# Optimization experiments

Measured on AMD Instinct MI355X. Metric: run time of the kernel, lower is better.

The kernel has to match this reference:

```python
import jax, jax.numpy as jnp
import numpy as np

B, SQ, SKV, D = 8, 2048, 2048, 1024

def setup_inputs() -> dict:
    key = jax.random.key(0)
    ks = jax.random.split(key, 8)
    s = 1.0 / np.sqrt(D)  # torch Linear default init range
    return {
        "target": jax.random.normal(ks[0], (B, SQ, D), dtype=jnp.float32),
        "non_target": jax.random.normal(ks[1], (B, SKV, D), dtype=jnp.float32),
        "Wq": jax.random.uniform(ks[2], (D, D), jnp.float32, -s, s),
        "bq": jax.random.uniform(ks[3], (D,), jnp.float32, -s, s),
        "Wk": jax.random.uniform(ks[4], (D, D), jnp.float32, -s, s),
        "bk": jax.random.uniform(ks[5], (D,), jnp.float32, -s, s),
        "Wv": jax.random.uniform(ks[6], (D, D), jnp.float32, -s, s),
        "bv": jax.random.uniform(ks[7], (D,), jnp.float32, -s, s),
    }

def reference(target, non_target, Wq, bq, Wk, bk, Wv, bv):
    # Linear projections (torch Linear: x @ W.T + b)
    q = jnp.einsum('bsd,ed->bse', target, Wq) + bq       # [B,SQ,D]
    k = jnp.einsum('bsd,ed->bse', non_target, Wk) + bk   # [B,SKV,D]
    v = jnp.einsum('bsd,ed->bse', non_target, Wv) + bv   # [B,SKV,D]
    # Unscaled attention, exactly as the original module (no 1/sqrt(d))
    scores = jnp.einsum('bqd,bkd->bqk', q, k)            # [B,SQ,SKV]
    weights = jax.nn.softmax(scores, axis=-1)
    return jnp.einsum('bqk,bkd->bqd', weights, v)        # [B,SQ,D]
```

## Files before the change

### kernel.cpp

```cpp
#include <hip/hip_runtime.h>


typedef _Float16 half8 __attribute__((ext_vector_type(8)));
typedef _Float16 half4v __attribute__((ext_vector_type(4)));
typedef float floatx4 __attribute__((ext_vector_type(4)));

__device__ __forceinline__ void async_copy16(const _Float16* g, _Float16* l) {
  __builtin_amdgcn_global_load_lds(
      (const __attribute__((address_space(1))) void*)g,
      (__attribute__((address_space(3))) void*)l,
      16, 0, 0);
}

__global__ __launch_bounds__(256) void cast_f32_f16(const float* __restrict__ src,
                                                    _Float16* __restrict__ dst, long n) {
  long i = ((long)blockIdx.x * 256 + threadIdx.x) * 8;
  if (i >= n) return;
  float4 a = *(const float4*)(src + i);
  float4 b = *(const float4*)(src + i + 4);
  half8 h;
  h[0] = (_Float16)a.x; h[1] = (_Float16)a.y; h[2] = (_Float16)a.z; h[3] = (_Float16)a.w;
  h[4] = (_Float16)b.x; h[5] = (_Float16)b.y; h[6] = (_Float16)b.z; h[7] = (_Float16)b.w;
  *(half8*)(dst + i) = h;
}

template <int OMODE>
__global__ __launch_bounds__(256, 2) void gemm_bt(const _Float16* __restrict__ A,
                                                  const _Float16* __restrict__ B,
                                                  const float* __restrict__ bias,
                                                  void* __restrict__ out,
                                                  int K, int N,
                                                  long sA, long sB, long sO) {
  __shared__ __attribute__((aligned(16))) _Float16 As[128 * 64];
  __shared__ __attribute__((aligned(16))) _Float16 Bs[128 * 64];

  const int tid = threadIdx.x;
  const int lane = tid & 63;
  const int wave = tid >> 6;
  const long bz = blockIdx.z;

  const _Float16* Ab = A + bz * sA + (long)blockIdx.x * 128 * K;
  const _Float16* Bb = B + bz * sB + (long)blockIdx.y * 128 * K;

  const int wm = (wave & 1) * 64;
  const int wn = (wave >> 1) * 64;
  const int frow = lane & 15;
  const int fq = lane >> 4;
  const int fsw = frow & 7;

  floatx4 acc[4][4];
#pragma unroll
  for (int mt = 0; mt < 4; mt++)
#pragma unroll
    for (int nt = 0; nt < 4; nt++)
      acc[mt][nt] = (floatx4){0.f, 0.f, 0.f, 0.f};

  const int sr = tid >> 3;
  const int gl = (tid & 7) ^ (sr & 7);
  const long gOffBase = (long)sr * K + gl * 8;
  const int ldsOff = tid * 8;

  for (int k0 = 0; k0 < K; k0 += 64) {
    __syncthreads();
#pragma unroll
    for (int j = 0; j < 4; j++) {
      async_copy16(Ab + gOffBase + (long)(32 * j) * K + k0, As + ldsOff + j * 2048);
      async_copy16(Bb + gOffBase + (long)(32 * j) * K + k0, Bs + ldsOff + j * 2048);
    }
    __syncthreads();

#pragma unroll
    for (int h = 0; h < 2; h++) {
      half8 af[4], bf[4];
#pragma unroll
      for (int mt = 0; mt < 4; mt++)
        af[mt] = *(const half8*)(As + (wm + mt * 16 + frow) * 64 + ((h * 4 + fq) ^ fsw) * 8);
#pragma unroll
      for (int nt = 0; nt < 4; nt++)
        bf[nt] = *(const half8*)(Bs + (wn + nt * 16 + frow) * 64 + ((h * 4 + fq) ^ fsw) * 8);
#pragma unroll
      for (int mt = 0; mt < 4; mt++)
#pragma unroll
        for (int nt = 0; nt < 4; nt++)
          acc[mt][nt] = __builtin_amdgcn_mfma_f32_16x16x32_f16(af[mt], bf[nt], acc[mt][nt], 0, 0, 0);
    }
  }

  if (OMODE == 2 || OMODE == 3) {
#pragma unroll
    for (int nt = 0; nt < 4; nt++) {
      const int n = blockIdx.y * 128 + wn + nt * 16 + frow;
#pragma unroll
      for (int mt = 0; mt < 4; mt++) {
        const int rbase = blockIdx.x * 128 + wm + mt * 16 + fq * 4;
#pragma unroll
        for (int i = 0; i < 4; i++) {
          if (OMODE == 2)
            ((float*)out + bz * sO)[(long)(rbase + i) * N + n] = acc[mt][nt][i];
          else
            ((_Float16*)out + bz * sO)[(long)(rbase + i) * N + n] = (_Float16)acc[mt][nt][i];
        }
      }
    }
  } else {
#pragma unroll
    for (int nt = 0; nt < 4; nt++) {
      const int n = blockIdx.y * 128 + wn + nt * 16 + frow;
      const float bvv = bias[n];
#pragma unroll
      for (int mt = 0; mt < 4; mt++) {
        const int rbase = blockIdx.x * 128 + wm + mt * 16 + fq * 4;
        if (OMODE == 0) {
#pragma unroll
          for (int i = 0; i < 4; i++)
            ((_Float16*)out)[(long)(rbase + i) * N + n] = (_Float16)(acc[mt][nt][i] + bvv);
        } else {
          const long bb = rbase >> 11;
          const int s = rbase & 2047;
          half4v hv;
#pragma unroll
          for (int i = 0; i < 4; i++) hv[i] = (_Float16)(acc[mt][nt][i] + bvv);
          *(half4v*)((_Float16*)out + bb * (2048l * 1024) + (long)n * 2048 + s) = hv;
        }
      }
    }
  }
}

__global__ __launch_bounds__(256) void softmax_rows(const _Float16* __restrict__ S,
                                                    _Float16* __restrict__ P) {
  const long row = blockIdx.x;
  const _Float16* src = S + row * 2048;
  _Float16* dst = P + row * 2048;
  const int tid = threadIdx.x;

  half8 v = ((const half8*)src)[tid];
  float f[8];
#pragma unroll
  for (int i = 0; i < 8; i++) f[i] = (float)v[i];

  float m = fmaxf(fmaxf(fmaxf(f[0], f[1]), fmaxf(f[2], f[3])),
                  fmaxf(fmaxf(f[4], f[5]), fmaxf(f[6], f[7])));
#pragma unroll
  for (int o = 32; o > 0; o >>= 1) m = fmaxf(m, __shfl_xor(m, o, 64));
  __shared__ float redm[4];
  if ((tid & 63) == 0) redm[tid >> 6] = m;
  __syncthreads();
  m = fmaxf(fmaxf(redm[0], redm[1]), fmaxf(redm[2], redm[3]));

  float e[8], s = 0.f;
#pragma unroll
  for (int i = 0; i < 8; i++) { e[i] = __expf(f[i] - m); s += e[i]; }
#pragma unroll
  for (int o = 32; o > 0; o >>= 1) s += __shfl_xor(s, o, 64);
  __shared__ float reds[4];
  if ((tid & 63) == 0) reds[tid >> 6] = s;
  __syncthreads();
  s = (reds[0] + reds[1]) + (reds[2] + reds[3]);
  const float inv = 1.f / s;

  half8 h;
#pragma unroll
  for (int i = 0; i < 8; i++) h[i] = (_Float16)(e[i] * inv);
  ((half8*)dst)[tid] = h;
}

extern "C" void kernel_launch(void* const* d_in, const int* in_sizes, int n_in,
                              void* d_out, int out_size, void* d_ws, size_t ws_size,
                              hipStream_t stream) {
  const float* target = (const float*)d_in[0];
  const float* non_target = (const float*)d_in[1];
  const float* Wq = (const float*)d_in[2];
  const float* bq = (const float*)d_in[3];
  const float* Wk = (const float*)d_in[4];
  const float* bk = (const float*)d_in[5];
  const float* Wv = (const float*)d_in[6];
  const float* bv = (const float*)d_in[7];

  char* ws = (char*)d_ws;
  const size_t MB = 1ull << 20;
  _Float16* tgt16 = (_Float16*)(ws);
  _Float16* ntg16 = (_Float16*)(ws + 32 * MB);
  _Float16* S16 = (_Float16*)(ws);
  _Float16* P16 = (_Float16*)(ws + 64 * MB);
  _Float16* Q16 = (_Float16*)(ws + 128 * MB);
  _Float16* K16 = (_Float16*)(ws + 160 * MB);
  _Float16* Vt16 = (_Float16*)(ws + 192 * MB);
  _Float16* Wq16 = (_Float16*)(ws + 224 * MB);
  _Float16* Wk16 = (_Float16*)(ws + 226 * MB);
  _Float16* Wv16 = (_Float16*)(ws + 228 * MB);

  const long nBig = 8l * 2048 * 1024;
  const long nW = 1024l * 1024;

  cast_f32_f16<<<8192, 256, 0, stream>>>(target, tgt16, nBig);
  cast_f32_f16<<<8192, 256, 0, stream>>>(non_target, ntg16, nBig);
  cast_f32_f16<<<512, 256, 0, stream>>>(Wq, Wq16, nW);
  cast_f32_f16<<<512, 256, 0, stream>>>(Wk, Wk16, nW);
  cast_f32_f16<<<512, 256, 0, stream>>>(Wv, Wv16, nW);

  gemm_bt<0><<<dim3(128, 8, 1), 256, 0, stream>>>(tgt16, Wq16, bq, Q16, 1024, 1024, 0, 0, 0);
  gemm_bt<0><<<dim3(128, 8, 1), 256, 0, stream>>>(ntg16, Wk16, bk, K16, 1024, 1024, 0, 0, 0);
  gemm_bt<1><<<dim3(128, 8, 1), 256, 0, stream>>>(ntg16, Wv16, bv, Vt16, 1024, 1024, 0, 0, 0);

  gemm_bt<3><<<dim3(16, 16, 8), 256, 0, stream>>>(Q16, K16, nullptr, S16, 1024, 2048,
                                                  2048l * 1024, 2048l * 1024, 2048l * 2048);

  softmax_rows<<<16384, 256, 0, stream>>>(S16, P16);

  gemm_bt<2><<<dim3(16, 8, 8), 256, 0, stream>>>(P16, Vt16, nullptr, (float*)d_out, 2048, 1024,
                                                 2048l * 2048, 1024l * 2048, 2048l * 1024);
}
```

Measured before the change: 477.5 us.

## Fuse fp32-to-fp16 input cast into QKV projection GEMM and batch launches

```diff
diff --git a/kernel.cpp b/kernel.cpp
--- a/kernel.cpp
+++ b/kernel.cpp
@@ -12,22 +12,135 @@
       16, 0, 0);
 }
 
-__global__ __launch_bounds__(256) void cast_f32_f16(const float* __restrict__ src,
-                                                    _Float16* __restrict__ dst, long n) {
+__global__ __launch_bounds__(256) void cast_w(const float* __restrict__ Wq,
+                                              const float* __restrict__ Wk,
+                                              const float* __restrict__ Wv,
+                                              _Float16* __restrict__ dst) {
+  const float* src = blockIdx.y == 0 ? Wq : (blockIdx.y == 1 ? Wk : Wv);
+  const long base = (long)blockIdx.y * (1024l * 1024);
   long i = ((long)blockIdx.x * 256 + threadIdx.x) * 8;
-  if (i >= n) return;
   float4 a = *(const float4*)(src + i);
   float4 b = *(const float4*)(src + i + 4);
   half8 h;
   h[0] = (_Float16)a.x; h[1] = (_Float16)a.y; h[2] = (_Float16)a.z; h[3] = (_Float16)a.w;
   h[4] = (_Float16)b.x; h[5] = (_Float16)b.y; h[6] = (_Float16)b.z; h[7] = (_Float16)b.w;
-  *(half8*)(dst + i) = h;
+  *(half8*)(dst + base + i) = h;
+}
+
+__global__ __launch_bounds__(256, 2) void proj_fused(
+    const float* __restrict__ tgt, const float* __restrict__ ntg,
+    const _Float16* __restrict__ Wall,
+    const float* __restrict__ bq, const float* __restrict__ bk, const float* __restrict__ bv,
+    _Float16* __restrict__ QK16, _Float16* __restrict__ Vt16) {
+  constexpr int K = 1024, N = 1024;
+  __shared__ __attribute__((aligned(16))) _Float16 As[128 * 64];
+  __shared__ __attribute__((aligned(16))) _Float16 Bs[128 * 64];
+
+  const int tid = threadIdx.x;
+  const int lane = tid & 63;
+  const int wave = tid >> 6;
+  const int by = blockIdx.y;
+  const int mblk = blockIdx.x >> 3;
+  const int nblk = blockIdx.x & 7;
+
+  const float* Ag = (by == 0 ? tgt : ntg) + (long)mblk * 128 * K;
+  const _Float16* Bb = Wall + (long)by * (K * N) + (long)nblk * 128 * K;
+  const float* bias = (by == 0) ? bq : (by == 1 ? bk : bv);
+
+  const int wm = (wave & 1) * 64;
+  const int wn = (wave >> 1) * 64;
+  const int frow = lane & 15;
+  const int fq = lane >> 4;
+  const int fsw = frow & 7;
+
+  floatx4 acc[4][4];
+#pragma unroll
+  for (int mt = 0; mt < 4; mt++)
+#pragma unroll
+    for (int nt = 0; nt < 4; nt++)
+      acc[mt][nt] = (floatx4){0.f, 0.f, 0.f, 0.f};
+
+  const int sr = tid >> 3;
+  const int gl = (tid & 7) ^ (sr & 7);
+  const long gOff = (long)sr * K + gl * 8;
+  const int ldsOff = tid * 8;
+
+  for (int k0 = 0; k0 < K; k0 += 64) {
+    __syncthreads();
+#pragma unroll
+    for (int j = 0; j < 4; j++)
+      async_copy16(Bb + gOff + (long)(32 * j) * K + k0, Bs + ldsOff + j * 2048);
+    float4 u[4], w[4];
+#pragma unroll
+    for (int j = 0; j < 4; j++) {
+      const float4* ap = (const float4*)(Ag + gOff + (long)(32 * j) * K + k0);
+      u[j] = ap[0];
+      w[j] = ap[1];
+    }
+#pragma unroll
+    for (int j = 0; j < 4; j++) {
+      half8 h;
+      h[0] = (_Float16)u[j].x; h[1] = (_Float16)u[j].y;
+      h[2] = (_Float16)u[j].z; h[3] = (_Float16)u[j].w;
+      h[4] = (_Float16)w[j].x; h[5] = (_Float16)w[j].y;
+      h[6] = (_Float16)w[j].z; h[7] = (_Float16)w[j].w;
+      *(half8*)(As + ldsOff + j * 2048) = h;
+    }
+    __syncthreads();
+
+#pragma unroll
+    for (int h = 0; h < 2; h++) {
+      half8 af[4], bf[4];
+#pragma unroll
+      for (int mt = 0; mt < 4; mt++)
+        af[mt] = *(const half8*)(As + (wm + mt * 16 + frow) * 64 + ((h * 4 + fq) ^ fsw) * 8);
+#pragma unroll
+      for (int nt = 0; nt < 4; nt++)
+        bf[nt] = *(const half8*)(Bs + (wn + nt * 16 + frow) * 64 + ((h * 4 + fq) ^ fsw) * 8);
+#pragma unroll
+      for (int mt = 0; mt < 4; mt++)
+#pragma unroll
+        for (int nt = 0; nt < 4; nt++)
+          acc[mt][nt] = __builtin_amdgcn_mfma_f32_16x16x32_f16(af[mt], bf[nt], acc[mt][nt], 0, 0, 0);
+    }
+  }
+
+  if (by != 2) {
+    _Float16* O = QK16 + (long)by * (16l * 1024 * 1024);
+#pragma unroll
+    for (int nt = 0; nt < 4; nt++) {
+      const int n = nblk * 128 + wn + nt * 16 + frow;
+      const float bvv = bias[n];
+#pragma unroll
+      for (int mt = 0; mt < 4; mt++) {
+        const int rbase = mblk * 128 + wm + mt * 16 + fq * 4;
+#pragma unroll
+        for (int i = 0; i < 4; i++)
+          O[(long)(rbase + i) * N + n] = (_Float16)(acc[mt][nt][i] + bvv);
+      }
+    }
+  } else {
+#pragma unroll
+    for (int nt = 0; nt < 4; nt++) {
+      const int n = nblk * 128 + wn + nt * 16 + frow;
+      const float bvv = bias[n];
+#pragma unroll
+      for (int mt = 0; mt < 4; mt++) {
+        const int rbase = mblk * 128 + wm + mt * 16 + fq * 4;
+        const long bb = rbase >> 11;
+        const int s = rbase & 2047;
+        half4v hv;
+#pragma unroll
+        for (int i = 0; i < 4; i++) hv[i] = (_Float16)(acc[mt][nt][i] + bvv);
+        *(half4v*)(Vt16 + bb * (2048l * 1024) + (long)n * 2048 + s) = hv;
+      }
+    }
+  }
 }
 
 template <int OMODE>
 __global__ __launch_bounds__(256, 2) void gemm_bt(const _Float16* __restrict__ A,
                                                   const _Float16* __restrict__ B,
-                                                  const float* __restrict__ bias,
                                                   void* __restrict__ out,
                                                   int K, int N,
                                                   long sA, long sB, long sO) {
@@ -86,42 +199,18 @@
     }
   }
 
-  if (OMODE == 2 || OMODE == 3) {
-#pragma unroll
-    for (int nt = 0; nt < 4; nt++) {
-      const int n = blockIdx.y * 128 + wn + nt * 16 + frow;
-#pragma unroll
-      for (int mt = 0; mt < 4; mt++) {
-        const int rbase = blockIdx.x * 128 + wm + mt * 16 + fq * 4;
-#pragma unroll
-        for (int i = 0; i < 4; i++) {
-          if (OMODE == 2)
-            ((float*)out + bz * sO)[(long)(rbase + i) * N + n] = acc[mt][nt][i];
-          else
-            ((_Float16*)out + bz * sO)[(long)(rbase + i) * N + n] = (_Float16)acc[mt][nt][i];
-        }
-      }
-    }
-  } else {
-#pragma unroll
-    for (int nt = 0; nt < 4; nt++) {
-      const int n = blockIdx.y * 128 + wn + nt * 16 + frow;
-      const float bvv = bias[n];
-#pragma unroll
-      for (int mt = 0; mt < 4; mt++) {
-        const int rbase = blockIdx.x * 128 + wm + mt * 16 + fq * 4;
-        if (OMODE == 0) {
-#pragma unroll
-          for (int i = 0; i < 4; i++)
-            ((_Float16*)out)[(long)(rbase + i) * N + n] = (_Float16)(acc[mt][nt][i] + bvv);
-        } else {
-          const long bb = rbase >> 11;
-          const int s = rbase & 2047;
-          half4v hv;
-#pragma unroll
-          for (int i = 0; i < 4; i++) hv[i] = (_Float16)(acc[mt][nt][i] + bvv);
-          *(half4v*)((_Float16*)out + bb * (2048l * 1024) + (long)n * 2048 + s) = hv;
-        }
+#pragma unroll
+  for (int nt = 0; nt < 4; nt++) {
+    const int n = blockIdx.y * 128 + wn + nt * 16 + frow;
+#pragma unroll
+    for (int mt = 0; mt < 4; mt++) {
+      const int rbase = blockIdx.x * 128 + wm + mt * 16 + fq * 4;
+#pragma unroll
+      for (int i = 0; i < 4; i++) {
+        if (OMODE == 2)
+          ((float*)out + bz * sO)[(long)(rbase + i) * N + n] = acc[mt][nt][i];
+        else
+          ((_Float16*)out + bz * sO)[(long)(rbase + i) * N + n] = (_Float16)acc[mt][nt][i];
       }
     }
   }
@@ -179,35 +268,23 @@
 
   char* ws = (char*)d_ws;
   const size_t MB = 1ull << 20;
-  _Float16* tgt16 = (_Float16*)(ws);
-  _Float16* ntg16 = (_Float16*)(ws + 32 * MB);
   _Float16* S16 = (_Float16*)(ws);
   _Float16* P16 = (_Float16*)(ws + 64 * MB);
   _Float16* Q16 = (_Float16*)(ws + 128 * MB);
-  _Float16* K16 = (_Float16*)(ws + 160 * MB);
   _Float16* Vt16 = (_Float16*)(ws + 192 * MB);
-  _Float16* Wq16 = (_Float16*)(ws + 224 * MB);
-  _Float16* Wk16 = (_Float16*)(ws + 226 * MB);
-  _Float16* Wv16 = (_Float16*)(ws + 228 * MB);
-
-  const long nBig = 8l * 2048 * 1024;
-  const long nW = 1024l * 1024;
-
-  cast_f32_f16<<<8192, 256, 0, stream>>>(target, tgt16, nBig);
-  cast_f32_f16<<<8192, 256, 0, stream>>>(non_target, ntg16, nBig);
-  cast_f32_f16<<<512, 256, 0, stream>>>(Wq, Wq16, nW);
-  cast_f32_f16<<<512, 256, 0, stream>>>(Wk, Wk16, nW);
-  cast_f32_f16<<<512, 256, 0, stream>>>(Wv, Wv16, nW);
-
-  gemm_bt<0><<<dim3(128, 8, 1), 256, 0, stream>>>(tgt16, Wq16, bq, Q16, 1024, 1024, 0, 0, 0);
-  gemm_bt<0><<<dim3(128, 8, 1), 256, 0, stream>>>(ntg16, Wk16, bk, K16, 1024, 1024, 0, 0, 0);
-  gemm_bt<1><<<dim3(128, 8, 1), 256, 0, stream>>>(ntg16, Wv16, bv, Vt16, 1024, 1024, 0, 0, 0);
-
-  gemm_bt<3><<<dim3(16, 16, 8), 256, 0, stream>>>(Q16, K16, nullptr, S16, 1024, 2048,
+  _Float16* W16 = (_Float16*)(ws + 224 * MB);
+  _Float16* K16 = Q16 + 16l * 1024 * 1024;
+
+  cast_w<<<dim3(512, 3), 256, 0, stream>>>(Wq, Wk, Wv, W16);
+
+  proj_fused<<<dim3(1024, 3), 256, 0, stream>>>(target, non_target, W16,
+                                                bq, bk, bv, Q16, Vt16);
+
+  gemm_bt<3><<<dim3(16, 16, 8), 256, 0, stream>>>(Q16, K16, S16, 1024, 2048,
                                                   2048l * 1024, 2048l * 1024, 2048l * 2048);
 
   softmax_rows<<<16384, 256, 0, stream>>>(S16, P16);
 
-  gemm_bt<2><<<dim3(16, 8, 8), 256, 0, stream>>>(P16, Vt16, nullptr, (float*)d_out, 2048, 1024,
+  gemm_bt<2><<<dim3(16, 8, 8), 256, 0, stream>>>(P16, Vt16, (float*)d_out, 2048, 1024,
                                                  2048l * 2048, 1024l * 2048, 2048l * 1024);
 }
```

Measured after the change: 551.5 us. +15.5%, slower.
